# Kernel tuning notes

Hardware: AMD Instinct MI355X
Metric: run time of the kernel (lower is better)

The kernel has to match this reference:

```python
import jax, jax.numpy as jnp
import numpy as np

N_NODES = 50000
N_EDGES = 800000
HEADS = 5
NFEAT = 5
C1 = 32  # hidden_layers


def setup_inputs() -> dict:
    key = jax.random.key(0)
    ks = jax.random.split(key, 20)
    s = 0.3  # glorot-ish scale
    d = {
        "x": jax.random.normal(ks[0], (N_NODES, NFEAT), jnp.float32),
        "edge_attr": jax.random.uniform(ks[1], (N_EDGES, 1), jnp.float32),
        "src": jax.random.randint(ks[2], (N_EDGES,), 0, N_NODES, jnp.int32),
        "dst": jax.random.randint(ks[3], (N_EDGES,), 0, N_NODES, jnp.int32),
        # conv1: in=5 -> heads=5, out=32, concat
        "W1": jax.random.normal(ks[4], (NFEAT, HEADS * C1), jnp.float32) * s,
        "a_src1": jax.random.normal(ks[5], (HEADS, C1), jnp.float32) * s,
        "a_dst1": jax.random.normal(ks[6], (HEADS, C1), jnp.float32) * s,
        "We1": jax.random.normal(ks[7], (1, HEADS * C1), jnp.float32) * s,
        "ae1": jax.random.normal(ks[8], (HEADS, C1), jnp.float32) * s,
        "b1": jnp.zeros((HEADS * C1,), jnp.float32),
        # conv2: in=160 -> heads=5, out=1, mean over heads
        "W2": jax.random.normal(ks[9], (HEADS * C1, HEADS * 1), jnp.float32) * 0.08,
        "a_src2": jax.random.normal(ks[10], (HEADS, 1), jnp.float32) * s,
        "a_dst2": jax.random.normal(ks[11], (HEADS, 1), jnp.float32) * s,
        "We2": jax.random.normal(ks[12], (1, HEADS * 1), jnp.float32) * s,
        "ae2": jax.random.normal(ks[13], (HEADS, 1), jnp.float32) * s,
        "b2": jnp.zeros((1,), jnp.float32),
        "Wlin": jax.random.normal(ks[14], (1, 1), jnp.float32),
    }
    return d


def gat_layer(x, src, dst, eattr, W, a_src, a_dst, We, a_e, bias, concat, n_nodes):
    """PyG GATConv with edge_dim, self-loops already added by caller."""
    H, C = a_src.shape
    h = (x @ W).reshape(-1, H, C)                      # [N,H,C]
    alpha_s = (h * a_src[None]).sum(-1)                # [N,H]
    alpha_d = (h * a_dst[None]).sum(-1)                # [N,H]
    ee = (eattr @ We).reshape(-1, H, C)                # [E,H,C]
    alpha_e = (ee * a_e[None]).sum(-1)                 # [E,H]
    logits = jax.nn.leaky_relu(alpha_s[src] + alpha_d[dst] + alpha_e, 0.2)
    # segment softmax over destination nodes
    m = jax.ops.segment_max(logits, dst, num_segments=n_nodes)
    m = jnp.where(jnp.isfinite(m), m, 0.0)
    ex = jnp.exp(logits - m[dst])
    denom = jax.ops.segment_sum(ex, dst, num_segments=n_nodes)
    alpha = ex / (denom[dst] + 1e-16)                  # [E,H]
    msg = (alpha[:, :, None] * h[src]).reshape(-1, H * C)
    agg = jax.ops.segment_sum(msg, dst, num_segments=n_nodes).reshape(n_nodes, H, C)
    if concat:
        return agg.reshape(n_nodes, H * C) + bias
    return agg.mean(axis=1) + bias


def reference(x, edge_attr, src, dst, W1, a_src1, a_dst1, We1, ae1, b1,
              W2, a_src2, a_dst2, We2, ae2, b2, Wlin):
    n = x.shape[0]
    loop = jnp.arange(n, dtype=src.dtype)
    s = jnp.concatenate([src, loop])
    t = jnp.concatenate([dst, loop])
    # self-loop edge_attr = mean of edge_attr (PyG fill_value='mean')
    ea_loop = jnp.broadcast_to(edge_attr.mean(axis=0, keepdims=True), (n, edge_attr.shape[1]))
    ea = jnp.concatenate([edge_attr, ea_loop], axis=0)

    x1 = gat_layer(x, s, t, ea, W1, a_src1, a_dst1, We1, ae1, b1, True, n)
    x2 = jax.nn.relu(x1)
    # dropout p=0.2 is identity in eval mode
    x4 = gat_layer(x2, s, t, ea, W2, a_src2, a_dst2, We2, ae2, b2, False, n)
    x5 = x4 @ Wlin                                     # Linear(1,1,bias=False)
    return jax.nn.sigmoid(x5)                          # [N,1]
```

## Files before the change

### kernel.cpp

```cpp
#include <hip/hip_runtime.h>
#include <hip/hip_fp16.h>
#include <math.h>

#define N_NODES 50000
#define N_EDGES 800000
#define E2 (N_EDGES + N_NODES)
#define HEADS 5
#define C1 32
#define F1 160

#define BSZ 64
#define NBK 782
#define NBL 128
#define CH  6641
#define MTOT (NBK*NBL)
#define MC  391
#define GRID_H1 (N_NODES/4)
#define CAP 1408

#define AGG1_NPB 32
#define AGG1_NB  1563

static constexpr size_t alignup(size_t x){ return (x + 255) & ~size_t(255); }
static constexpr size_t OFF_SCAL  = 0;
static constexpr size_t OFF_H     = alignup(OFF_SCAL + 64*4);
static constexpr size_t OFF_EAS   = alignup(OFF_H    + (size_t)MTOT*4);
static constexpr size_t OFF_PART  = alignup(OFF_EAS  + (size_t)NBL*4);
static constexpr size_t OFF_PPREF = alignup(OFF_PART + (size_t)MC*4);
static constexpr size_t OFF_BST   = alignup(OFF_PPREF+ (size_t)MC*4);
static constexpr size_t OFF_OFFS  = alignup(OFF_BST  + (size_t)(NBK+1)*4);
static constexpr size_t OFF_BPACK = alignup(OFF_OFFS + (size_t)(N_NODES+1)*4);
static constexpr size_t OFF_EDG   = alignup(OFF_BPACK+ (size_t)E2*8);
static constexpr size_t OFF_AS16  = alignup(OFF_EDG  + (size_t)E2*4);
static constexpr size_t OFF_AD16  = alignup(OFF_AS16 + (size_t)N_NODES*8*2);
static constexpr size_t OFF_G16   = alignup(OFF_AD16 + (size_t)N_NODES*8*2);
static constexpr size_t OFF_AD2P  = alignup(OFF_G16  + (size_t)N_NODES*16*2);
static constexpr size_t OFF_H1Q   = alignup(OFF_AD2P + (size_t)N_NODES*8*4);
static constexpr size_t OFF_X2H   = alignup(OFF_H1Q  + (size_t)N_NODES*F1);
static constexpr size_t OFF_P2    = alignup(OFF_X2H  + (size_t)N_NODES*F1*2);

typedef float vf2 __attribute__((ext_vector_type(2)));
__device__ __forceinline__ float4 fp8x4_to_f32(unsigned int r){
  vf2 lo = __builtin_amdgcn_cvt_pk_f32_fp8((int)r, false);
  vf2 hi = __builtin_amdgcn_cvt_pk_f32_fp8((int)r, true);
  return make_float4(lo.x, lo.y, hi.x, hi.y);
}

__global__ __launch_bounds__(320) void k_init(const float* __restrict__ x, const float* __restrict__ W1,
                       const float* __restrict__ as1w, const float* __restrict__ ad1w,
                       unsigned short* __restrict__ h1qh, __half* __restrict__ as16, __half* __restrict__ ad16,
                       const int* __restrict__ dst, const float* __restrict__ ea,
                       int* __restrict__ H, float* __restrict__ easum){
  __shared__ float sW[5*F1];
  int t = threadIdx.x;
  if (blockIdx.x < GRID_H1){
    for (int k = t; k < 5*F1; k += 320) sW[k] = W1[k];
    __syncthreads();
    int nl = t / 80;
    int c  = t - nl*80;
    int n  = blockIdx.x*4 + nl;
    int c0 = 2*c;
    float hv0 = 0.f, hv1 = 0.f;
    #pragma unroll
    for (int f = 0; f < 5; f++){
      float xv = x[n*5 + f];
      hv0 += xv * sW[f*F1 + c0];
      hv1 += xv * sW[f*F1 + c0 + 1];
    }
    int pk = __builtin_amdgcn_cvt_pk_fp8_f32(hv0, hv1, 0, false);
    int hh = c >> 4, pp = c & 15;
    h1qh[(size_t)hh*(N_NODES*16) + n*16 + pp] = (unsigned short)(pk & 0xFFFF);
    float vs = hv0*as1w[c0] + hv1*as1w[c0+1];
    float vd = hv0*ad1w[c0] + hv1*ad1w[c0+1];
    #pragma unroll
    for (int m = 8; m >= 1; m >>= 1){
      vs += __shfl_xor(vs, m, 64);
      vd += __shfl_xor(vd, m, 64);
    }
    if ((c & 15) == 0){
      int h = c >> 4;
      as16[n*8 + h] = __float2half(vs);
      ad16[n*8 + h] = __float2half(vd);
    }
  } else {
    int* hist = (int*)sW;
    float* wsum = (float*)&hist[NBK + 1];
    for (int k = t; k < NBK; k += 320) hist[k] = 0;
    __syncthreads();
    int b = blockIdx.x - GRID_H1;
    int e0 = b*CH, e1 = min(e0 + CH, E2);
    float s = 0.f;
    for (int e = e0 + t; e < e1; e += 320){
      int d;
      if (e < N_EDGES){ d = dst[e]; s += ea[e]; }
      else d = e - N_EDGES;
      atomicAdd(&hist[d >> 6], 1);
    }
    #pragma unroll
    for (int m = 1; m < 64; m <<= 1) s += __shfl_xor(s, m, 64);
    if ((t & 63) == 0) wsum[t >> 6] = s;
    __syncthreads();
    for (int k = t; k < NBK; k += 320) H[(size_t)k*NBL + b] = hist[k];
    if (t == 0) easum[b] = wsum[0] + wsum[1] + wsum[2] + wsum[3] + wsum[4];
  }
}

__global__ void k_s1(const int* __restrict__ H, int* __restrict__ partial){
  int i = blockIdx.x*256 + threadIdx.x;
  int v = (i < MTOT) ? H[i] : 0;
  #pragma unroll
  for (int m = 1; m < 64; m <<= 1) v += __shfl_xor(v, m, 64);
  __shared__ int sh[4];
  if ((threadIdx.x & 63) == 0) sh[threadIdx.x >> 6] = v;
  __syncthreads();
  if (threadIdx.x == 0) partial[blockIdx.x] = sh[0] + sh[1] + sh[2] + sh[3];
}

__global__ __launch_bounds__(512) void k_s2p(const int* __restrict__ partial, int* __restrict__ ppref,
                      int* __restrict__ offs, int* __restrict__ bstart,
                      const float* __restrict__ easum,
                      const float* __restrict__ We1, const float* __restrict__ ae1,
                      const float* __restrict__ We2, const float* __restrict__ ae2,
                      float* __restrict__ scal){
  __shared__ int sp[512];
  __shared__ float sh_ea[NBL];
  int t = threadIdx.x;
  if (t < NBL) sh_ea[t] = easum[t];
  if (t >= 448 && t < 448 + HEADS){
    int h = t - 448;
    float s = 0.f;
    for (int c = 0; c < C1; c++) s += We1[h*C1 + c] * ae1[h*C1 + c];
    scal[2 + h] = s;
    scal[7 + h] = We2[h] * ae2[h];
  }
  int v = (t < MC) ? partial[t] : 0;
  sp[t] = v;
  __syncthreads();
  if (t == 511){
    float es = 0.f;
    for (int i = 0; i < NBL; i++) es += sh_ea[i];
    scal[1] = es / (float)N_EDGES;
  }
  for (int off = 1; off < 512; off <<= 1){
    int u = (t >= off) ? sp[t - off] : 0;
    __syncthreads();
    sp[t] += u;
    __syncthreads();
  }
  if (t < MC) ppref[t] = sp[t] - v;
  if (t == 0){ offs[N_NODES] = E2; bstart[NBK] = E2; }
}

__global__ void k_s3(int* __restrict__ H, const int* __restrict__ ppref, int* __restrict__ bstart){
  __shared__ int sp[256];
  int b = blockIdx.x, t = threadIdx.x;
  int i = b*256 + t;
  int v = (i < MTOT) ? H[i] : 0;
  sp[t] = v;
  __syncthreads();
  for (int off = 1; off < 256; off <<= 1){
    int u = (t >= off) ? sp[t - off] : 0;
    __syncthreads();
    sp[t] += u;
    __syncthreads();
  }
  int P = ppref[b] + sp[t] - v;
  if (i < MTOT){
    H[i] = P;
    if (i % NBL == 0) bstart[i / NBL] = P;
  }
}

__global__ __launch_bounds__(256) void k_scat(const int* __restrict__ src, const int* __restrict__ dst,
                       const float* __restrict__ ea, const float* __restrict__ scal,
                       const int* __restrict__ H, int2* __restrict__ bpack){
  __shared__ int lofs[NBK];
  int b = blockIdx.x;
  for (int k = threadIdx.x; k < NBK; k += 256) lofs[k] = H[(size_t)k*NBL + b];
  __syncthreads();
  float mean = scal[1];
  int e0 = b*CH, e1 = min(e0 + CH, E2);
  for (int e = e0 + threadIdx.x; e < e1; e += 256){
    int d, s; float a;
    if (e < N_EDGES){ d = dst[e]; s = src[e]; a = ea[e]; }
    else { d = s = e - N_EDGES; a = mean; }
    int pos = atomicAdd(&lofs[d >> 6], 1);
    bpack[pos] = make_int2(s | ((d & 63) << 16), __float_as_int(a));
  }
}

__global__ __launch_bounds__(256) void k_final2(const int* __restrict__ bstart,
                        const int2* __restrict__ bpack,
                        int* __restrict__ offs, unsigned int* __restrict__ edge2){
  __shared__ int cnt[BSZ], cur[BSZ];
  __shared__ unsigned int s_edge[CAP];
  int k = blockIdx.x, t = threadIdx.x;
  int base = k*BSZ;
  if (t < BSZ) cnt[t] = 0;
  __syncthreads();
  int r0 = bstart[k], r1 = bstart[k + 1];
  int sz = r1 - r0;
  for (int j = r0 + t; j < r1; j += 256) atomicAdd(&cnt[(bpack[j].x >> 16) & 63], 1);
  __syncthreads();
  if (t == 0){
    int run = 0;
    for (int i = 0; i < BSZ; i++){ int c = cnt[i]; cnt[i] = run; cur[i] = run; run += c; }
  }
  __syncthreads();
  if (t < BSZ){
    int n = base + t;
    if (n < N_NODES) offs[n] = r0 + cnt[t];
  }
  if (sz <= CAP){
    for (int j = r0 + t; j < r1; j += 256){
      int2 v = bpack[j];
      int lp = atomicAdd(&cur[(v.x >> 16) & 63], 1);
      s_edge[lp] = (unsigned int)(v.x & 0xFFFF) |
                   ((unsigned int)__half_as_ushort(__float2half(__int_as_float(v.y))) << 16);
    }
    __syncthreads();
    for (int i = t; i < sz; i += 256) edge2[r0 + i] = s_edge[i];
  } else {
    for (int j = r0 + t; j < r1; j += 256){
      int2 v = bpack[j];
      int pos = r0 + atomicAdd(&cur[(v.x >> 16) & 63], 1);
      edge2[pos] = (unsigned int)(v.x & 0xFFFF) |
                   ((unsigned int)__half_as_ushort(__float2half(__int_as_float(v.y))) << 16);
    }
  }
}

__global__ __launch_bounds__(256) void k_logit(const int* __restrict__ offs,
                      const unsigned int* __restrict__ edge2,
                      const __half* __restrict__ as16, const __half* __restrict__ ad16,
                      const float* __restrict__ scal,
                      unsigned int* __restrict__ P01, unsigned int* __restrict__ P2){
  int gl = threadIdx.x >> 3;
  int q  = threadIdx.x & 7;
  int n  = blockIdx.x*AGG1_NPB + gl;
  if (n >= N_NODES) return;
  union { uint4 u; __half2 h[4]; } AD; AD.u = *(const uint4*)(ad16 + (size_t)n*8);
  float ad0 = __low2float(AD.h[0]), ad1 = __high2float(AD.h[0]);
  float ad2 = __low2float(AD.h[1]), ad3 = __high2float(AD.h[1]);
  float ad4 = __low2float(AD.h[2]);
  float wd0 = scal[2], wd1 = scal[3], wd2 = scal[4], wd3 = scal[5], wd4 = scal[6];
  int j0 = offs[n], j1 = offs[n + 1];
  for (int j = j0 + q; j < j1; j += 8){
    unsigned int e = edge2[j];
    unsigned int lo = e & 0xFFFFu;
    int s = (int)lo;
    float c = __half2float(__ushort_as_half((unsigned short)(e >> 16)));
    union { uint4 u; __half2 h[4]; } AS; AS.u = *(const uint4*)(as16 + (size_t)s*8);
    float l0 = __low2float(AS.h[0])  + ad0 + c*wd0;  l0 = fminf(fmaxf(l0, 0.2f*l0), 10.f);
    float l1 = __high2float(AS.h[0]) + ad1 + c*wd1;  l1 = fminf(fmaxf(l1, 0.2f*l1), 10.f);
    float l2 = __low2float(AS.h[1])  + ad2 + c*wd2;  l2 = fminf(fmaxf(l2, 0.2f*l2), 10.f);
    float l3 = __high2float(AS.h[1]) + ad3 + c*wd3;  l3 = fminf(fmaxf(l3, 0.2f*l3), 10.f);
    float l4 = __low2float(AS.h[2])  + ad4 + c*wd4;  l4 = fminf(fmaxf(l4, 0.2f*l4), 10.f);
    unsigned int p0 = (unsigned int)__half_as_ushort(__float2half(__expf(l0)));
    unsigned int p1 = (unsigned int)__half_as_ushort(__float2half(__expf(l1)));
    unsigned int p2 = (unsigned int)__half_as_ushort(__float2half(__expf(l2)));
    unsigned int p3 = (unsigned int)__half_as_ushort(__float2half(__expf(l3)));
    unsigned int p4 = (unsigned int)__half_as_ushort(__float2half(__expf(l4)));
    P01[j]                  = lo | (p0 << 16);
    P01[(size_t)E2 + j]     = lo | (p1 << 16);
    P2[j]                   = lo | (p2 << 16);
    P2[(size_t)E2 + j]      = lo | (p3 << 16);
    P2[(size_t)2*E2 + j]    = lo | (p4 << 16);
  }
}

__global__ __launch_bounds__(256) void k_agg1(const int* __restrict__ offs,
                      const unsigned int* __restrict__ P01, const unsigned int* __restrict__ P2,
                      const unsigned short* __restrict__ h1qh,
                      const float* __restrict__ b1, __half* __restrict__ x2h){
  int head = blockIdx.x / AGG1_NB;
  int nb   = blockIdx.x - head*AGG1_NB;
  int gl   = threadIdx.x >> 3;
  int q    = threadIdx.x & 7;
  int n    = nb*AGG1_NPB + gl;
  if (n >= N_NODES) return;
  const unsigned int* EP = (head < 2) ? (P01 + (size_t)head*E2)
                                      : (P2  + (size_t)(head-2)*E2);
  const unsigned int* h1row = (const unsigned int*)h1qh + (size_t)head*(N_NODES*8) + q;
  int j0 = offs[n], j1 = offs[n + 1];
  float a0 = 0.f, a1 = 0.f, a2 = 0.f, a3 = 0.f, den = 0.f;
  int j = j0;
  for (; j + 7 < j1; j += 8){
    uint4 sa = *(const uint4*)(EP + j);
    uint4 sb = *(const uint4*)(EP + j + 4);
    unsigned int e0 = sa.x, e1 = sa.y, e2v = sa.z, e3 = sa.w;
    unsigned int e4 = sb.x, e5 = sb.y, e6 = sb.z, e7 = sb.w;
    int s0 = e0 & 0xFFFF, s1 = e1 & 0xFFFF, s2 = e2v & 0xFFFF, s3 = e3 & 0xFFFF;
    int s4 = e4 & 0xFFFF, s5 = e5 & 0xFFFF, s6 = e6 & 0xFFFF, s7 = e7 & 0xFFFF;
    unsigned int r0 = h1row[s0*8];
    unsigned int r1 = h1row[s1*8];
    unsigned int r2 = h1row[s2*8];
    unsigned int r3 = h1row[s3*8];
    unsigned int r4 = h1row[s4*8];
    unsigned int r5 = h1row[s5*8];
    unsigned int r6 = h1row[s6*8];
    unsigned int r7 = h1row[s7*8];
    float p0 = __half2float(__ushort_as_half((unsigned short)(e0 >> 16)));
    float p1 = __half2float(__ushort_as_half((unsigned short)(e1 >> 16)));
    float p2 = __half2float(__ushort_as_half((unsigned short)(e2v >> 16)));
    float p3 = __half2float(__ushort_as_half((unsigned short)(e3 >> 16)));
    float p4 = __half2float(__ushort_as_half((unsigned short)(e4 >> 16)));
    float p5 = __half2float(__ushort_as_half((unsigned short)(e5 >> 16)));
    float p6 = __half2float(__ushort_as_half((unsigned short)(e6 >> 16)));
    float p7 = __half2float(__ushort_as_half((unsigned short)(e7 >> 16)));
    den += ((p0 + p1) + (p2 + p3)) + ((p4 + p5) + (p6 + p7));
    float4 f0 = fp8x4_to_f32(r0), f1 = fp8x4_to_f32(r1);
    float4 f2 = fp8x4_to_f32(r2), f3 = fp8x4_to_f32(r3);
    float4 f4 = fp8x4_to_f32(r4), f5 = fp8x4_to_f32(r5);
    float4 f6 = fp8x4_to_f32(r6), f7 = fp8x4_to_f32(r7);
    a0 += p0*f0.x; a1 += p0*f0.y; a2 += p0*f0.z; a3 += p0*f0.w;
    a0 += p1*f1.x; a1 += p1*f1.y; a2 += p1*f1.z; a3 += p1*f1.w;
    a0 += p2*f2.x; a1 += p2*f2.y; a2 += p2*f2.z; a3 += p2*f2.w;
    a0 += p3*f3.x; a1 += p3*f3.y; a2 += p3*f3.z; a3 += p3*f3.w;
    a0 += p4*f4.x; a1 += p4*f4.y; a2 += p4*f4.z; a3 += p4*f4.w;
    a0 += p5*f5.x; a1 += p5*f5.y; a2 += p5*f5.z; a3 += p5*f5.w;
    a0 += p6*f6.x; a1 += p6*f6.y; a2 += p6*f6.z; a3 += p6*f6.w;
    a0 += p7*f7.x; a1 += p7*f7.y; a2 += p7*f7.z; a3 += p7*f7.w;
  }
  for (; j < j1; ++j){
    unsigned int e = EP[j];
    int s = e & 0xFFFF;
    float p = __half2float(__ushort_as_half((unsigned short)(e >> 16)));
    den += p;
    float4 f = fp8x4_to_f32(h1row[s*8]);
    a0 += p*f.x; a1 += p*f.y; a2 += p*f.z; a3 += p*f.w;
  }
  float inv = 1.f / (den + 1e-16f);
  float4 bb = *(const float4*)(b1 + head*C1 + 4*q);
  float v0 = fmaxf(a0*inv + bb.x, 0.f);
  float v1 = fmaxf(a1*inv + bb.y, 0.f);
  float v2 = fmaxf(a2*inv + bb.z, 0.f);
  float v3 = fmaxf(a3*inv + bb.w, 0.f);
  __half2 o0 = __floats2half2_rn(v0, v1);
  __half2 o1 = __floats2half2_rn(v2, v3);
  *(uint2*)(x2h + (size_t)n*F1 + head*C1 + 4*q) =
      make_uint2(*(unsigned int*)&o0, *(unsigned int*)&o1);
}

__global__ __launch_bounds__(256) void k_h2(const __half* __restrict__ x2h, const float* __restrict__ W2,
                    const float* __restrict__ asw2, const float* __restrict__ adw2,
                    __half* __restrict__ G16, float* __restrict__ ad2p){
  __shared__ float sW[F1*HEADS];
  for (int k = threadIdx.x; k < F1*HEADS; k += 256) sW[k] = W2[k];
  __syncthreads();
  int w = threadIdx.x >> 6, l = threadIdx.x & 63;
  int n = blockIdx.x*4 + w;
  const __half2* x22 = (const __half2*)x2h;
  float acc[HEADS] = {0.f, 0.f, 0.f, 0.f, 0.f};
  for (int k2 = l; k2 < 80; k2 += 64){
    float2 f = __half22float2(x22[(size_t)n*80 + k2]);
    #pragma unroll
    for (int h = 0; h < HEADS; h++)
      acc[h] += f.x * sW[(2*k2)*HEADS + h] + f.y * sW[(2*k2+1)*HEADS + h];
  }
  #pragma unroll
  for (int m = 1; m < 64; m <<= 1){
    #pragma unroll
    for (int h = 0; h < HEADS; h++) acc[h] += __shfl_xor(acc[h], m, 64);
  }
  if (l == 0){
    #pragma unroll
    for (int h = 0; h < HEADS; h++){
      G16[(size_t)n*16 + h]     = __float2half(acc[h]);
      G16[(size_t)n*16 + 5 + h] = __float2half(acc[h] * asw2[h]);
      ad2p[n*8 + h]             = acc[h] * adw2[h];
    }
    #pragma unroll
    for (int z = 10; z < 16; z++) G16[(size_t)n*16 + z] = __float2half(0.f);
  }
}

__global__ __launch_bounds__(256) void k_agg2(const int* __restrict__ offs,
                      const unsigned int* __restrict__ edge2,
                      const __half* __restrict__ G16, const float* __restrict__ ad2p,
                      const float* __restrict__ scal,
                      const float* __restrict__ b2, const float* __restrict__ Wlin,
                      float* __restrict__ out){
  int grp = threadIdx.x >> 4;
  int l16 = threadIdx.x & 15;
  int n = blockIdx.x*16 + grp;
  float adn[HEADS], wd[HEADS];
  #pragma unroll
  for (int h = 0; h < HEADS; h++){ adn[h] = ad2p[n*8 + h]; wd[h] = scal[7 + h]; }
  int j0 = offs[n], j1 = offs[n + 1];

  float den[HEADS] = {0,0,0,0,0};
  float ac[HEADS]  = {0,0,0,0,0};
  for (int j = j0 + l16; j < j1; j += 16){
    unsigned int e = edge2[j];
    int s = e & 0xFFFF;
    float c = __half2float(__ushort_as_half((unsigned short)(e >> 16)));
    const __half* gs = G16 + (size_t)s*16;
    union { uint4 u; __half2 h[4]; } U; U.u = *(const uint4*)gs;
    union { uint2 u; __half2 h[2]; } V; V.u = *(const uint2*)(gs + 8);
    float2 p01 = __half22float2(U.h[0]);
    float2 p23 = __half22float2(U.h[1]);
    float2 p45 = __half22float2(U.h[2]);
    float2 p67 = __half22float2(U.h[3]);
    float2 p89 = __half22float2(V.h[0]);
    float hv[HEADS] = {p01.x, p01.y, p23.x, p23.y, p45.x};
    float av[HEADS] = {p45.y, p67.x, p67.y, p89.x, p89.y};
    #pragma unroll
    for (int h = 0; h < HEADS; h++){
      float lg = av[h] + adn[h] + c*wd[h];
      lg = fmaxf(lg, 0.2f*lg);
      lg = fminf(lg, 50.f);
      float p = __expf(lg);
      den[h] += p;
      ac[h]  += p * hv[h];
    }
  }
  #pragma unroll
  for (int m = 1; m < 16; m <<= 1){
    #pragma unroll
    for (int h = 0; h < HEADS; h++){
      den[h] += __shfl_xor(den[h], m, 16);
      ac[h]  += __shfl_xor(ac[h], m, 16);
    }
  }
  if (l16 == 0){
    float v = 0.f;
    #pragma unroll
    for (int h = 0; h < HEADS; h++) v += ac[h] / (den[h] + 1e-16f);
    v = v * (1.f/HEADS) + b2[0];
    v *= Wlin[0];
    out[n] = 1.f / (1.f + __expf(-v));
  }
}

extern "C" void kernel_launch(void* const* d_in, const int* in_sizes, int n_in,
                              void* d_out, int out_size, void* d_ws, size_t ws_size,
                              hipStream_t stream) {
  const float* x    = (const float*)d_in[0];
  const float* ea   = (const float*)d_in[1];
  const int*   src  = (const int*)d_in[2];
  const int*   dst  = (const int*)d_in[3];
  const float* W1   = (const float*)d_in[4];
  const float* as1w = (const float*)d_in[5];
  const float* ad1w = (const float*)d_in[6];
  const float* We1  = (const float*)d_in[7];
  const float* ae1  = (const float*)d_in[8];
  const float* b1   = (const float*)d_in[9];
  const float* W2   = (const float*)d_in[10];
  const float* as2w = (const float*)d_in[11];
  const float* ad2w = (const float*)d_in[12];
  const float* We2  = (const float*)d_in[13];
  const float* ae2  = (const float*)d_in[14];
  const float* b2   = (const float*)d_in[15];
  const float* Wlin = (const float*)d_in[16];

  char* ws = (char*)d_ws;
  float* scal   = (float*)(ws + OFF_SCAL);
  int*   H      = (int*)  (ws + OFF_H);
  float* easum  = (float*)(ws + OFF_EAS);
  int*   part   = (int*)  (ws + OFF_PART);
  int*   ppref  = (int*)  (ws + OFF_PPREF);
  int*   bstart = (int*)  (ws + OFF_BST);
  int*   offs   = (int*)  (ws + OFF_OFFS);
  int2*  bpack  = (int2*) (ws + OFF_BPACK);
  unsigned int* P01 = (unsigned int*)(ws + OFF_BPACK);
  unsigned int* P2  = (unsigned int*)(ws + OFF_P2);
  unsigned int* edge2 = (unsigned int*)(ws + OFF_EDG);
  __half* as16  = (__half*)(ws + OFF_AS16);
  __half* ad16  = (__half*)(ws + OFF_AD16);
  __half* G16   = (__half*)(ws + OFF_G16);
  float* ad2p   = (float*)(ws + OFF_AD2P);
  unsigned short* h1qh = (unsigned short*)(ws + OFF_H1Q);
  __half* x2h   = (__half*)(ws + OFF_X2H);
  float* outp   = (float*)d_out;

  k_init   <<<GRID_H1 + NBL, 320, 0, stream>>>(x, W1, as1w, ad1w, h1qh, as16, ad16,
                                               dst, ea, H, easum);
  k_s1     <<<MC, 256, 0, stream>>>(H, part);
  k_s2p    <<<1, 512, 0, stream>>>(part, ppref, offs, bstart, easum, We1, ae1, We2, ae2, scal);
  k_s3     <<<MC, 256, 0, stream>>>(H, ppref, bstart);
  k_scat   <<<NBL, 256, 0, stream>>>(src, dst, ea, scal, H, bpack);
  k_final2 <<<NBK, 256, 0, stream>>>(bstart, bpack, offs, edge2);

  k_logit  <<<AGG1_NB, 256, 0, stream>>>(offs, edge2, as16, ad16, scal, P01, P2);
  k_agg1   <<<HEADS*AGG1_NB, 256, 0, stream>>>(offs, P01, P2, h1qh, b1, x2h);
  k_h2     <<<N_NODES/4, 256, 0, stream>>>(x2h, W2, as2w, ad2w, G16, ad2p);
  k_agg2   <<<N_NODES/16, 256, 0, stream>>>(offs, edge2, G16, ad2p, scal, b2, Wlin, outp);
}
```

Baseline: 224.1 us.

## Fuse logit computation into CSR build and fold W2 projection into agg1

The edge-logit/exp computation moves into k_final2, so edges are processed right after the CSR reorder instead of being reread in a separate k_logit pass, and P01/P2 now get their own buffers rather than aliasing bpack. k_agg1 now multiplies its ReLU output slice by the matching W2 rows and atomically accumulates per-node layer-2 projections into h2acc, which k_s1 zeroes. A small k_h2b kernel then packs G16 and ad2p. This removes the fp16 x2h intermediate and the k_h2 reduction pass, at the cost of float atomics (5 heads contend per node), a nondeterministic summation order, and a larger workspace.

Result: faster. 209.3 us (-6.6%).

```diff
diff --git a/kernel.cpp b/kernel.cpp
--- a/kernel.cpp
+++ b/kernel.cpp
@@ -36,8 +36,9 @@
 static constexpr size_t OFF_G16   = alignup(OFF_AD16 + (size_t)N_NODES*8*2);
 static constexpr size_t OFF_AD2P  = alignup(OFF_G16  + (size_t)N_NODES*16*2);
 static constexpr size_t OFF_H1Q   = alignup(OFF_AD2P + (size_t)N_NODES*8*4);
-static constexpr size_t OFF_X2H   = alignup(OFF_H1Q  + (size_t)N_NODES*F1);
-static constexpr size_t OFF_P2    = alignup(OFF_X2H  + (size_t)N_NODES*F1*2);
+static constexpr size_t OFF_P01   = alignup(OFF_H1Q  + (size_t)N_NODES*F1);
+static constexpr size_t OFF_P2    = alignup(OFF_P01  + (size_t)2*E2*4);
+static constexpr size_t OFF_H2A   = alignup(OFF_P2   + (size_t)3*E2*4);
 
 typedef float vf2 __attribute__((ext_vector_type(2)));
 __device__ __forceinline__ float4 fp8x4_to_f32(unsigned int r){
@@ -105,8 +106,10 @@
   }
 }
 
-__global__ void k_s1(const int* __restrict__ H, int* __restrict__ partial){
+__global__ void k_s1(const int* __restrict__ H, int* __restrict__ partial,
+                     float* __restrict__ h2acc){
   int i = blockIdx.x*256 + threadIdx.x;
+  for (int z = i; z < N_NODES*HEADS; z += MC*256) h2acc[z] = 0.f;
   int v = (i < MTOT) ? H[i] : 0;
   #pragma unroll
   for (int m = 1; m < 64; m <<= 1) v += __shfl_xor(v, m, 64);
@@ -191,12 +194,26 @@
 
 __global__ __launch_bounds__(256) void k_final2(const int* __restrict__ bstart,
                         const int2* __restrict__ bpack,
-                        int* __restrict__ offs, unsigned int* __restrict__ edge2){
+                        const __half* __restrict__ as16, const __half* __restrict__ ad16,
+                        const float* __restrict__ scal,
+                        int* __restrict__ offs, unsigned int* __restrict__ edge2,
+                        unsigned int* __restrict__ P01, unsigned int* __restrict__ P2){
   __shared__ int cnt[BSZ], cur[BSZ];
   __shared__ unsigned int s_edge[CAP];
+  __shared__ unsigned char s_d6[CAP];
+  __shared__ float sAd[HEADS][BSZ];
   int k = blockIdx.x, t = threadIdx.x;
   int base = k*BSZ;
-  if (t < BSZ) cnt[t] = 0;
+  if (t < BSZ){
+    cnt[t] = 0;
+    int n = base + t;
+    uint4 adu = make_uint4(0,0,0,0);
+    if (n < N_NODES) adu = *(const uint4*)(ad16 + (size_t)n*8);
+    union { uint4 u; __half2 h[4]; } AD; AD.u = adu;
+    sAd[0][t] = __low2float(AD.h[0]); sAd[1][t] = __high2float(AD.h[0]);
+    sAd[2][t] = __low2float(AD.h[1]); sAd[3][t] = __high2float(AD.h[1]);
+    sAd[4][t] = __low2float(AD.h[2]);
+  }
   __syncthreads();
   int r0 = bstart[k], r1 = bstart[k + 1];
   int sz = r1 - r0;
@@ -211,70 +228,77 @@
     int n = base + t;
     if (n < N_NODES) offs[n] = r0 + cnt[t];
   }
+  float wd0 = scal[2], wd1 = scal[3], wd2 = scal[4], wd3 = scal[5], wd4 = scal[6];
   if (sz <= CAP){
     for (int j = r0 + t; j < r1; j += 256){
       int2 v = bpack[j];
-      int lp = atomicAdd(&cur[(v.x >> 16) & 63], 1);
+      int d6 = (v.x >> 16) & 63;
+      int lp = atomicAdd(&cur[d6], 1);
       s_edge[lp] = (unsigned int)(v.x & 0xFFFF) |
                    ((unsigned int)__half_as_ushort(__float2half(__int_as_float(v.y))) << 16);
-    }
-    __syncthreads();
-    for (int i = t; i < sz; i += 256) edge2[r0 + i] = s_edge[i];
+      s_d6[lp] = (unsigned char)d6;
+    }
+    __syncthreads();
+    for (int i = t; i < sz; i += 256){
+      unsigned int e = s_edge[i];
+      unsigned int lo = e & 0xFFFFu;
+      int s = (int)lo;
+      int d6 = s_d6[i];
+      float c = __half2float(__ushort_as_half((unsigned short)(e >> 16)));
+      union { uint4 u; __half2 h[4]; } AS; AS.u = *(const uint4*)(as16 + (size_t)s*8);
+      float l0 = __low2float(AS.h[0])  + sAd[0][d6] + c*wd0;  l0 = fminf(fmaxf(l0, 0.2f*l0), 10.f);
+      float l1 = __high2float(AS.h[0]) + sAd[1][d6] + c*wd1;  l1 = fminf(fmaxf(l1, 0.2f*l1), 10.f);
+      float l2 = __low2float(AS.h[1])  + sAd[2][d6] + c*wd2;  l2 = fminf(fmaxf(l2, 0.2f*l2), 10.f);
+      float l3 = __high2float(AS.h[1]) + sAd[3][d6] + c*wd3;  l3 = fminf(fmaxf(l3, 0.2f*l3), 10.f);
+      float l4 = __low2float(AS.h[2])  + sAd[4][d6] + c*wd4;  l4 = fminf(fmaxf(l4, 0.2f*l4), 10.f);
+      unsigned int p0 = (unsigned int)__half_as_ushort(__float2half(__expf(l0)));
+      unsigned int p1 = (unsigned int)__half_as_ushort(__float2half(__expf(l1)));
+      unsigned int p2 = (unsigned int)__half_as_ushort(__float2half(__expf(l2)));
+      unsigned int p3 = (unsigned int)__half_as_ushort(__float2half(__expf(l3)));
+      unsigned int p4 = (unsigned int)__half_as_ushort(__float2half(__expf(l4)));
+      int pos = r0 + i;
+      edge2[pos]               = e;
+      P01[pos]                 = lo | (p0 << 16);
+      P01[(size_t)E2 + pos]    = lo | (p1 << 16);
+      P2[pos]                  = lo | (p2 << 16);
+      P2[(size_t)E2 + pos]     = lo | (p3 << 16);
+      P2[(size_t)2*E2 + pos]   = lo | (p4 << 16);
+    }
   } else {
     for (int j = r0 + t; j < r1; j += 256){
       int2 v = bpack[j];
-      int pos = r0 + atomicAdd(&cur[(v.x >> 16) & 63], 1);
-      edge2[pos] = (unsigned int)(v.x & 0xFFFF) |
-                   ((unsigned int)__half_as_ushort(__float2half(__int_as_float(v.y))) << 16);
-    }
-  }
-}
-
-__global__ __launch_bounds__(256) void k_logit(const int* __restrict__ offs,
-                      const unsigned int* __restrict__ edge2,
-                      const __half* __restrict__ as16, const __half* __restrict__ ad16,
-                      const float* __restrict__ scal,
-                      unsigned int* __restrict__ P01, unsigned int* __restrict__ P2){
-  int gl = threadIdx.x >> 3;
-  int q  = threadIdx.x & 7;
-  int n  = blockIdx.x*AGG1_NPB + gl;
-  if (n >= N_NODES) return;
-  union { uint4 u; __half2 h[4]; } AD; AD.u = *(const uint4*)(ad16 + (size_t)n*8);
-  float ad0 = __low2float(AD.h[0]), ad1 = __high2float(AD.h[0]);
-  float ad2 = __low2float(AD.h[1]), ad3 = __high2float(AD.h[1]);
-  float ad4 = __low2float(AD.h[2]);
-  float wd0 = scal[2], wd1 = scal[3], wd2 = scal[4], wd3 = scal[5], wd4 = scal[6];
-  int j0 = offs[n], j1 = offs[n + 1];
-  for (int j = j0 + q; j < j1; j += 8){
-    unsigned int e = edge2[j];
-    unsigned int lo = e & 0xFFFFu;
-    int s = (int)lo;
-    float c = __half2float(__ushort_as_half((unsigned short)(e >> 16)));
-    union { uint4 u; __half2 h[4]; } AS; AS.u = *(const uint4*)(as16 + (size_t)s*8);
-    float l0 = __low2float(AS.h[0])  + ad0 + c*wd0;  l0 = fminf(fmaxf(l0, 0.2f*l0), 10.f);
-    float l1 = __high2float(AS.h[0]) + ad1 + c*wd1;  l1 = fminf(fmaxf(l1, 0.2f*l1), 10.f);
-    float l2 = __low2float(AS.h[1])  + ad2 + c*wd2;  l2 = fminf(fmaxf(l2, 0.2f*l2), 10.f);
-    float l3 = __high2float(AS.h[1]) + ad3 + c*wd3;  l3 = fminf(fmaxf(l3, 0.2f*l3), 10.f);
-    float l4 = __low2float(AS.h[2])  + ad4 + c*wd4;  l4 = fminf(fmaxf(l4, 0.2f*l4), 10.f);
-    unsigned int p0 = (unsigned int)__half_as_ushort(__float2half(__expf(l0)));
-    unsigned int p1 = (unsigned int)__half_as_ushort(__float2half(__expf(l1)));
-    unsigned int p2 = (unsigned int)__half_as_ushort(__float2half(__expf(l2)));
-    unsigned int p3 = (unsigned int)__half_as_ushort(__float2half(__expf(l3)));
-    unsigned int p4 = (unsigned int)__half_as_ushort(__float2half(__expf(l4)));
-    P01[j]                  = lo | (p0 << 16);
-    P01[(size_t)E2 + j]     = lo | (p1 << 16);
-    P2[j]                   = lo | (p2 << 16);
-    P2[(size_t)E2 + j]      = lo | (p3 << 16);
-    P2[(size_t)2*E2 + j]    = lo | (p4 << 16);
+      int d6 = (v.x >> 16) & 63;
+      int pos = r0 + atomicAdd(&cur[d6], 1);
+      int s = v.x & 0xFFFF;
+      float c = __int_as_float(v.y);
+      unsigned int lo = (unsigned int)s;
+      unsigned int e = lo | ((unsigned int)__half_as_ushort(__float2half(c)) << 16);
+      union { uint4 u; __half2 h[4]; } AS; AS.u = *(const uint4*)(as16 + (size_t)s*8);
+      float l0 = __low2float(AS.h[0])  + sAd[0][d6] + c*wd0;  l0 = fminf(fmaxf(l0, 0.2f*l0), 10.f);
+      float l1 = __high2float(AS.h[0]) + sAd[1][d6] + c*wd1;  l1 = fminf(fmaxf(l1, 0.2f*l1), 10.f);
+      float l2 = __low2float(AS.h[1])  + sAd[2][d6] + c*wd2;  l2 = fminf(fmaxf(l2, 0.2f*l2), 10.f);
+      float l3 = __high2float(AS.h[1]) + sAd[3][d6] + c*wd3;  l3 = fminf(fmaxf(l3, 0.2f*l3), 10.f);
+      float l4 = __low2float(AS.h[2])  + sAd[4][d6] + c*wd4;  l4 = fminf(fmaxf(l4, 0.2f*l4), 10.f);
+      edge2[pos]               = e;
+      P01[pos]                 = lo | ((unsigned int)__half_as_ushort(__float2half(__expf(l0))) << 16);
+      P01[(size_t)E2 + pos]    = lo | ((unsigned int)__half_as_ushort(__float2half(__expf(l1))) << 16);
+      P2[pos]                  = lo | ((unsigned int)__half_as_ushort(__float2half(__expf(l2))) << 16);
+      P2[(size_t)E2 + pos]     = lo | ((unsigned int)__half_as_ushort(__float2half(__expf(l3))) << 16);
+      P2[(size_t)2*E2 + pos]   = lo | ((unsigned int)__half_as_ushort(__float2half(__expf(l4))) << 16);
+    }
   }
 }
 
 __global__ __launch_bounds__(256) void k_agg1(const int* __restrict__ offs,
                       const unsigned int* __restrict__ P01, const unsigned int* __restrict__ P2,
                       const unsigned short* __restrict__ h1qh,
-                      const float* __restrict__ b1, __half* __restrict__ x2h){
+                      const float* __restrict__ b1, const float* __restrict__ W2,
+                      float* __restrict__ h2acc){
   int head = blockIdx.x / AGG1_NB;
   int nb   = blockIdx.x - head*AGG1_NB;
+  __shared__ float sW2[C1*HEADS];
+  for (int i = threadIdx.x; i < C1*HEADS; i += 256) sW2[i] = W2[head*C1*HEADS + i];
+  __syncthreads();
   int gl   = threadIdx.x >> 3;
   int q    = threadIdx.x & 7;
   int n    = nb*AGG1_NPB + gl;
@@ -336,43 +360,48 @@
   float v1 = fmaxf(a1*inv + bb.y, 0.f);
   float v2 = fmaxf(a2*inv + bb.z, 0.f);
   float v3 = fmaxf(a3*inv + bb.w, 0.f);
-  __half2 o0 = __floats2half2_rn(v0, v1);
-  __half2 o1 = __floats2half2_rn(v2, v3);
-  *(uint2*)(x2h + (size_t)n*F1 + head*C1 + 4*q) =
-      make_uint2(*(unsigned int*)&o0, *(unsigned int*)&o1);
-}
-
-__global__ __launch_bounds__(256) void k_h2(const __half* __restrict__ x2h, const float* __restrict__ W2,
+  const float* wr = sW2 + (4*q)*HEADS;
+  float hh[HEADS];
+  #pragma unroll
+  for (int h2i = 0; h2i < HEADS; h2i++)
+    hh[h2i] = v0*wr[0*HEADS + h2i] + v1*wr[1*HEADS + h2i]
+            + v2*wr[2*HEADS + h2i] + v3*wr[3*HEADS + h2i];
+  #pragma unroll
+  for (int m = 1; m < 8; m <<= 1){
+    #pragma unroll
+    for (int h2i = 0; h2i < HEADS; h2i++) hh[h2i] += __shfl_xor(hh[h2i], m, 8);
+  }
+  if (q == 0){
+    #pragma unroll
+    for (int h2i = 0; h2i < HEADS; h2i++)
+      atomicAdd(&h2acc[n*HEADS + h2i], hh[h2i]);
+  }
+}
+
+__global__ __launch_bounds__(256) void k_h2b(const float* __restrict__ h2acc,
                     const float* __restrict__ asw2, const float* __restrict__ adw2,
                     __half* __restrict__ G16, float* __restrict__ ad2p){
-  __shared__ float sW[F1*HEADS];
-  for (int k = threadIdx.x; k < F1*HEADS; k += 256) sW[k] = W2[k];
-  __syncthreads();
-  int w = threadIdx.x >> 6, l = threadIdx.x & 63;
-  int n = blockIdx.x*4 + w;
-  const __half2* x22 = (const __half2*)x2h;
-  float acc[HEADS] = {0.f, 0.f, 0.f, 0.f, 0.f};
-  for (int k2 = l; k2 < 80; k2 += 64){
-    float2 f = __half22float2(x22[(size_t)n*80 + k2]);
-    #pragma unroll
-    for (int h = 0; h < HEADS; h++)
-      acc[h] += f.x * sW[(2*k2)*HEADS + h] + f.y * sW[(2*k2+1)*HEADS + h];
-  }
-  #pragma unroll
-  for (int m = 1; m < 64; m <<= 1){
-    #pragma unroll
-    for (int h = 0; h < HEADS; h++) acc[h] += __shfl_xor(acc[h], m, 64);
-  }
-  if (l == 0){
-    #pragma unroll
-    for (int h = 0; h < HEADS; h++){
-      G16[(size_t)n*16 + h]     = __float2half(acc[h]);
-      G16[(size_t)n*16 + 5 + h] = __float2half(acc[h] * asw2[h]);
-      ad2p[n*8 + h]             = acc[h] * adw2[h];
-    }
-    #pragma unroll
-    for (int z = 10; z < 16; z++) G16[(size_t)n*16 + z] = __float2half(0.f);
-  }
+  int n = blockIdx.x*256 + threadIdx.x;
+  if (n >= N_NODES) return;
+  float a0 = h2acc[n*HEADS + 0], a1 = h2acc[n*HEADS + 1], a2 = h2acc[n*HEADS + 2];
+  float a3 = h2acc[n*HEADS + 3], a4 = h2acc[n*HEADS + 4];
+  float s0 = asw2[0], s1 = asw2[1], s2 = asw2[2], s3 = asw2[3], s4 = asw2[4];
+  __half2 g0 = __floats2half2_rn(a0, a1);
+  __half2 g1 = __floats2half2_rn(a2, a3);
+  __half2 g2 = __floats2half2_rn(a4, a0*s0);
+  __half2 g3 = __floats2half2_rn(a1*s1, a2*s2);
+  __half2 g4 = __floats2half2_rn(a3*s3, a4*s4);
+  __half2 z  = __floats2half2_rn(0.f, 0.f);
+  uint4 lo = make_uint4(*(unsigned int*)&g0, *(unsigned int*)&g1,
+                        *(unsigned int*)&g2, *(unsigned int*)&g3);
+  uint4 hi = make_uint4(*(unsigned int*)&g4, *(unsigned int*)&z,
+                        *(unsigned int*)&z,  *(unsigned int*)&z);
+  *(uint4*)(G16 + (size_t)n*16)     = lo;
+  *(uint4*)(G16 + (size_t)n*16 + 8) = hi;
+  float4 d0 = make_float4(a0*adw2[0], a1*adw2[1], a2*adw2[2], a3*adw2[3]);
+  float4 d1 = make_float4(a4*adw2[4], 0.f, 0.f, 0.f);
+  *(float4*)(ad2p + (size_t)n*8)     = d0;
+  *(float4*)(ad2p + (size_t)n*8 + 4) = d1;
 }
 
 __global__ __launch_bounds__(256) void k_agg2(const int* __restrict__ offs,
@@ -463,27 +492,26 @@
   int*   bstart = (int*)  (ws + OFF_BST);
   int*   offs   = (int*)  (ws + OFF_OFFS);
   int2*  bpack  = (int2*) (ws + OFF_BPACK);
-  unsigned int* P01 = (unsigned int*)(ws + OFF_BPACK);
+  unsigned int* edge2 = (unsigned int*)(ws + OFF_EDG);
+  unsigned int* P01 = (unsigned int*)(ws + OFF_P01);
   unsigned int* P2  = (unsigned int*)(ws + OFF_P2);
-  unsigned int* edge2 = (unsigned int*)(ws + OFF_EDG);
   __half* as16  = (__half*)(ws + OFF_AS16);
   __half* ad16  = (__half*)(ws + OFF_AD16);
   __half* G16   = (__half*)(ws + OFF_G16);
   float* ad2p   = (float*)(ws + OFF_AD2P);
   unsigned short* h1qh = (unsigned short*)(ws + OFF_H1Q);
-  __half* x2h   = (__half*)(ws + OFF_X2H);
+  float* h2acc  = (float*)(ws + OFF_H2A);
   float* outp   = (float*)d_out;
 
   k_init   <<<GRID_H1 + NBL, 320, 0, stream>>>(x, W1, as1w, ad1w, h1qh, as16, ad16,
                                                dst, ea, H, easum);
-  k_s1     <<<MC, 256, 0, stream>>>(H, part);
+  k_s1     <<<MC, 256, 0, stream>>>(H, part, h2acc);
   k_s2p    <<<1, 512, 0, stream>>>(part, ppref, offs, bstart, easum, We1, ae1, We2, ae2, scal);
   k_s3     <<<MC, 256, 0, stream>>>(H, ppref, bstart);
   k_scat   <<<NBL, 256, 0, stream>>>(src, dst, ea, scal, H, bpack);
-  k_final2 <<<NBK, 256, 0, stream>>>(bstart, bpack, offs, edge2);
-
-  k_logit  <<<AGG1_NB, 256, 0, stream>>>(offs, edge2, as16, ad16, scal, P01, P2);
-  k_agg1   <<<HEADS*AGG1_NB, 256, 0, stream>>>(offs, P01, P2, h1qh, b1, x2h);
-  k_h2     <<<N_NODES/4, 256, 0, stream>>>(x2h, W2, as2w, ad2w, G16, ad2p);
+  k_final2 <<<NBK, 256, 0, stream>>>(bstart, bpack, as16, ad16, scal, offs, edge2, P01, P2);
+
+  k_agg1   <<<HEADS*AGG1_NB, 256, 0, stream>>>(offs, P01, P2, h1qh, b1, W2, h2acc);
+  k_h2b    <<<(N_NODES + 255)/256, 256, 0, stream>>>(h2acc, as2w, ad2w, G16, ad2p);
   k_agg2   <<<N_NODES/16, 256, 0, stream>>>(offs, edge2, G16, ad2p, scal, b2, Wlin, outp);
 }
```
